# Kernel optimization log

Hardware: AMD Instinct MI355X
Metric: run time of the kernel (lower is better)

## Reference

```python
import jax, jax.numpy as jnp
import numpy as np

N_NODES = 100000
N_EDGES = 1600000
NUM_GRAPHS = 2000
IN_CH, HID = 5, 64
NEG_SLOPE = 0.2


def _lin_params(key, out_d, in_d, bias=True):
    k1, k2 = jax.random.split(key)
    bound = 1.0 / np.sqrt(in_d)
    W = jax.random.uniform(k1, (out_d, in_d), jnp.float32, -bound, bound)
    if bias:
        b = jax.random.uniform(k2, (out_d,), jnp.float32, -bound, bound)
        return W, b
    return (W,)


def setup_inputs() -> dict:
    key = jax.random.key(0)
    ks = jax.random.split(key, 12)
    x = jax.random.normal(ks[0], (N_NODES, IN_CH), jnp.float32)
    edge_index = jax.random.randint(ks[1], (2, N_EDGES), 0, N_NODES, jnp.int64)
    batch = (jnp.arange(N_NODES, dtype=jnp.int64) * NUM_GRAPHS) // N_NODES  # 50 nodes/graph, sorted
    # SAGEConv params: lin_l (on aggregated neighbors, with bias), lin_r (root, no bias)
    W1l, b1 = _lin_params(ks[2], HID, IN_CH)
    (W1r,) = _lin_params(ks[3], HID, IN_CH, bias=False)
    W2l, b2 = _lin_params(ks[4], 2 * HID, HID)
    (W2r,) = _lin_params(ks[5], 2 * HID, HID, bias=False)
    W3l, b3 = _lin_params(ks[6], 4 * HID, 2 * HID)
    (W3r,) = _lin_params(ks[7], 4 * HID, 2 * HID, bias=False)
    # classifier MLP: 512 -> 128 -> 64 -> 1
    Wc1, bc1 = _lin_params(ks[8], 2 * HID, 8 * HID)
    Wc2, bc2 = _lin_params(ks[9], HID, 2 * HID)
    Wc3, bc3 = _lin_params(ks[10], 1, HID)
    return {
        "x": x, "edge_index": edge_index, "batch": batch, "num_graphs": NUM_GRAPHS,
        "W1l": W1l, "b1": b1, "W1r": W1r,
        "W2l": W2l, "b2": b2, "W2r": W2r,
        "W3l": W3l, "b3": b3, "W3r": W3r,
        "Wc1": Wc1, "bc1": bc1, "Wc2": Wc2, "bc2": bc2, "Wc3": Wc3, "bc3": bc3,
    }


def _sage_conv(x, src, dst, Wl, b, Wr):
    # mean-aggregate messages x[src] at dst, then lin_l(agg) + lin_r(x)
    n = x.shape[0]
    s = jax.ops.segment_sum(x[src], dst, num_segments=n)
    cnt = jax.ops.segment_sum(jnp.ones((src.shape[0],), x.dtype), dst, num_segments=n)
    mean = s / jnp.maximum(cnt, 1.0)[:, None]
    return mean @ Wl.T + b + x @ Wr.T


def reference(x, edge_index, batch, num_graphs,
              W1l, b1, W1r, W2l, b2, W2r, W3l, b3, W3r,
              Wc1, bc1, Wc2, bc2, Wc3, bc3):
    src, dst = edge_index[0], edge_index[1]
    lrelu = lambda h: jax.nn.leaky_relu(h, NEG_SLOPE)
    h = lrelu(_sage_conv(x, src, dst, W1l, b1, W1r))
    h = lrelu(_sage_conv(h, src, dst, W2l, b2, W2r))
    h = lrelu(_sage_conv(h, src, dst, W3l, b3, W3r))
    # global mean + max pool per graph -> [G, 512]
    s = jax.ops.segment_sum(h, batch, num_segments=num_graphs)
    cnt = jax.ops.segment_sum(jnp.ones((h.shape[0],), h.dtype), batch, num_segments=num_graphs)
    mean_p = s / jnp.maximum(cnt, 1.0)[:, None]
    max_p = jax.ops.segment_max(h, batch, num_segments=num_graphs)
    g = jnp.concatenate([mean_p, max_p], axis=1)
    # classifier (dropout = identity in eval mode)
    g = lrelu(g @ Wc1.T + bc1)
    g = lrelu(g @ Wc2.T + bc2)
    logits = g @ Wc3.T + bc3
    return logits.squeeze(-1)
```

## Files before the change

kernel.cpp:

```cpp
#include <hip/hip_runtime.h>
#include <cstdint>
#include <cstddef>

#define NEG_SLOPE 0.2f

typedef __attribute__((ext_vector_type(8))) short bh8;
typedef __attribute__((ext_vector_type(16))) float f32x16;

__device__ inline void splitf(float x, short& hi, short& lo) {
    uint32_t u = __float_as_uint(x);
    uint32_t rh = (u + 0x7FFFu + ((u >> 16) & 1u)) & 0xFFFF0000u;
    hi = (short)(rh >> 16);
    float rem = x - __uint_as_float(rh);
    uint32_t u2 = __float_as_uint(rem);
    lo = (short)((u2 + 0x7FFFu + ((u2 >> 16) & 1u)) >> 16);
}

__device__ inline unsigned short f2bf(float x) {
    uint32_t u = __float_as_uint(x);
    return (unsigned short)((u + 0x7FFFu + ((u >> 16) & 1u)) >> 16);
}

__global__ void sentinel_kernel(float* __restrict__ out, int n) {
    int i = blockIdx.x * blockDim.x + threadIdx.x;
    if (i < n) out[i] = 12345.0f;
}

#define HIST_CH 8192
__global__ void bucket_count_kernel(const int* __restrict__ dst, int* __restrict__ bcnt,
                                    int ne, int nb) {
    __shared__ int hist[256];
    const int tid = threadIdx.x;
    hist[tid] = 0;
    __syncthreads();
    int e0 = blockIdx.x * HIST_CH;
    for (int i = tid; i < HIST_CH; i += 256) {
        int e = e0 + i;
        if (e < ne) atomicAdd(&hist[dst[e] >> 9], 1);
    }
    __syncthreads();
    if (tid < nb && hist[tid] > 0) atomicAdd(&bcnt[tid], hist[tid]);
}

__global__ void scan256_kernel(const int* __restrict__ bcnt, int* __restrict__ boff, int n) {
    const int tid = threadIdx.x, lane = tid & 63, wid = tid >> 6;
    __shared__ int wt[4];
    int v = (tid < n) ? bcnt[tid] : 0;
    int incl = v;
    #pragma unroll
    for (int o = 1; o < 64; o <<= 1) {
        int t = __shfl_up(incl, o);
        if (lane >= o) incl += t;
    }
    if (lane == 63) wt[wid] = incl;
    __syncthreads();
    if (tid < 4) {
        int w = wt[tid], winc = w;
        #pragma unroll
        for (int o = 1; o < 4; o <<= 1) {
            int t = __shfl_up(winc, o);
            if (tid >= o) winc += t;
        }
        wt[tid] = winc - w;
    }
    __syncthreads();
    int excl = wt[wid] + incl - v;
    if (tid < n) boff[tid] = excl;
    if (tid == n - 1) boff[n] = excl + v;
}

#define SCAT_CH 4096
__global__ void bucket_scatter_kernel(const int* __restrict__ src, const int* __restrict__ dst,
                                      const int* __restrict__ boff, int* __restrict__ bcur,
                                      unsigned* __restrict__ pairs, int ne, int nb) {
    __shared__ int hist[256], lcur[256], gbase[256];
    const int tid = threadIdx.x;
    hist[tid] = 0; lcur[tid] = 0;
    __syncthreads();
    int e0 = blockIdx.x * SCAT_CH;
    for (int i = tid; i < SCAT_CH; i += 256) {
        int e = e0 + i;
        if (e < ne) atomicAdd(&hist[dst[e] >> 9], 1);
    }
    __syncthreads();
    if (tid < nb) {
        int h = hist[tid];
        gbase[tid] = (h > 0) ? (boff[tid] + atomicAdd(&bcur[tid], h)) : 0;
    }
    __syncthreads();
    for (int i = tid; i < SCAT_CH; i += 256) {
        int e = e0 + i;
        if (e < ne) {
            int d = dst[e];
            int b = d >> 9;
            int r = atomicAdd(&lcur[b], 1);
            pairs[gbase[b] + r] = ((unsigned)(d & 511) << 17) | (unsigned)src[e];
        }
    }
}

__global__ __launch_bounds__(512) void bucket_sort_kernel(
        const unsigned* __restrict__ pairs, const int* __restrict__ boff,
        int* __restrict__ off, int* __restrict__ csr, int n_nodes) {
    __shared__ int cnt[512], lcur[512];
    __shared__ int wt[8];
    const int b = blockIdx.x;
    const int tid = threadIdx.x, lane = tid & 63, wid = tid >> 6;
    const int s = boff[b], t = boff[b + 1];
    cnt[tid] = 0; lcur[tid] = 0;
    __syncthreads();
    for (int i = s + tid; i < t; i += 512)
        atomicAdd(&cnt[pairs[i] >> 17], 1);
    __syncthreads();
    int v = cnt[tid];
    int incl = v;
    #pragma unroll
    for (int o = 1; o < 64; o <<= 1) {
        int tt = __shfl_up(incl, o);
        if (lane >= o) incl += tt;
    }
    if (lane == 63) wt[wid] = incl;
    __syncthreads();
    if (tid < 8) {
        int w = wt[tid], winc = w;
        #pragma unroll
        for (int o = 1; o < 8; o <<= 1) {
            int tt = __shfl_up(winc, o);
            if (tid >= o) winc += tt;
        }
        wt[tid] = winc - w;
    }
    __syncthreads();
    int excl = wt[wid] + incl - v;
    __syncthreads();
    cnt[tid] = excl;
    int node = b * 512 + tid;
    if (node < n_nodes) off[node] = s + excl;
    if (b == 0 && tid == 0) off[n_nodes] = boff[gridDim.x];
    __syncthreads();
    for (int i = s + tid; i < t; i += 512) {
        unsigned p = pairs[i];
        int bin = p >> 17;
        int r = atomicAdd(&lcur[bin], 1);
        csr[s + cnt[bin] + r] = (int)(p & 0x1FFFFu);
    }
}

__global__ void pack_wsplit_kernel(const float* __restrict__ Wl, const float* __restrict__ Wr,
                                   short* __restrict__ Whi, short* __restrict__ Wlo,
                                   int COUT, int K, int CIN) {
    int i = blockIdx.x * blockDim.x + threadIdx.x;
    if (i >= COUT * K) return;
    int n = i / K, k = i % K;
    float v = (k < CIN) ? Wl[n * CIN + k] : Wr[n * CIN + (k - CIN)];
    short h, l;
    splitf(v, h, l);
    Whi[i] = h; Wlo[i] = l;
}

__global__ __launch_bounds__(256) void sage1_kernel(
        const float* __restrict__ x, const int* __restrict__ off,
        const int* __restrict__ csr, const float* __restrict__ W1l,
        const float* __restrict__ W1r, const float* __restrict__ b1,
        float* __restrict__ h1, unsigned short* __restrict__ h1b, int n_nodes) {
    __shared__ float sWl[320], sWr[320], sb[64];
    const int tid = threadIdx.x;
    for (int i = tid; i < 320; i += 256) { sWl[i] = W1l[i]; sWr[i] = W1r[i]; }
    if (tid < 64) sb[tid] = b1[tid];
    __syncthreads();
    int node = blockIdx.x * 4 + (tid >> 6);
    int lane = tid & 63;
    if (node >= n_nodes) return;
    int slot = lane >> 3, cg = lane & 7;
    int e0 = off[node], cnt = off[node + 1] - e0;
    float a0 = 0.f, a1 = 0.f;
    int i = slot;
    for (; i + 8 < cnt; i += 16) {
        int s0 = csr[e0 + i];
        int s1 = csr[e0 + i + 8];
        a0 += (cg < 5) ? x[(size_t)s0 * 5 + cg] : 0.f;
        a1 += (cg < 5) ? x[(size_t)s1 * 5 + cg] : 0.f;
    }
    for (; i < cnt; i += 8) {
        int s = csr[e0 + i];
        a0 += (cg < 5) ? x[(size_t)s * 5 + cg] : 0.f;
    }
    float acc = a0 + a1;
    #pragma unroll
    for (int o = 8; o < 64; o <<= 1) acc += __shfl_xor(acc, o);
    float inv = (cnt > 0) ? 1.f / (float)cnt : 0.f;
    float m = acc * inv;
    float xv = (lane < 5) ? x[(size_t)node * 5 + lane] : 0.f;
    float o = sb[lane];
    #pragma unroll
    for (int c = 0; c < 5; ++c) {
        o += sWl[lane * 5 + c] * __shfl(m, c);
        o += sWr[lane * 5 + c] * __shfl(xv, c);
    }
    o = o > 0.f ? o : o * NEG_SLOPE;
    h1[(size_t)node * 64 + lane] = o;
    h1b[(size_t)node * 64 + lane] = f2bf(o);
}

template<int CIN>
__global__ void agg_bf16_kernel(const unsigned short* __restrict__ hb,
                                const int* __restrict__ off, const int* __restrict__ csr,
                                float* __restrict__ mean, int n_nodes) {
    constexpr int LPR = CIN / 8;
    constexpr int SLOTS = 64 / LPR;
    constexpr int UN = 16 / SLOTS;
    int node = blockIdx.x * (blockDim.x >> 6) + (threadIdx.x >> 6);
    int lane = threadIdx.x & 63;
    if (node >= n_nodes) return;
    int slot = lane / LPR, cg = lane % LPR;
    int e0 = off[node], cnt = off[node + 1] - e0;
    const unsigned short* base = hb + cg * 8;
    float acc[UN][8];
    #pragma unroll
    for (int u = 0; u < UN; ++u)
        #pragma unroll
        for (int k = 0; k < 8; ++k) acc[u][k] = 0.f;
    int i = slot;
    for (; i + (UN - 1) * SLOTS < cnt; i += UN * SLOTS) {
        int s[UN];
        #pragma unroll
        for (int u = 0; u < UN; ++u) s[u] = csr[e0 + i + u * SLOTS];
        uint4 v[UN];
        #pragma unroll
        for (int u = 0; u < UN; ++u)
            v[u] = *(const uint4*)(base + (size_t)s[u] * CIN);
        #pragma unroll
        for (int u = 0; u < UN; ++u) {
            unsigned w0 = v[u].x, w1 = v[u].y, w2 = v[u].z, w3 = v[u].w;
            acc[u][0] += __uint_as_float(w0 << 16);
            acc[u][1] += __uint_as_float(w0 & 0xFFFF0000u);
            acc[u][2] += __uint_as_float(w1 << 16);
            acc[u][3] += __uint_as_float(w1 & 0xFFFF0000u);
            acc[u][4] += __uint_as_float(w2 << 16);
            acc[u][5] += __uint_as_float(w2 & 0xFFFF0000u);
            acc[u][6] += __uint_as_float(w3 << 16);
            acc[u][7] += __uint_as_float(w3 & 0xFFFF0000u);
        }
    }
    for (; i < cnt; i += SLOTS) {
        uint4 v = *(const uint4*)(base + (size_t)csr[e0 + i] * CIN);
        unsigned w0 = v.x, w1 = v.y, w2 = v.z, w3 = v.w;
        acc[0][0] += __uint_as_float(w0 << 16);
        acc[0][1] += __uint_as_float(w0 & 0xFFFF0000u);
        acc[0][2] += __uint_as_float(w1 << 16);
        acc[0][3] += __uint_as_float(w1 & 0xFFFF0000u);
        acc[0][4] += __uint_as_float(w2 << 16);
        acc[0][5] += __uint_as_float(w2 & 0xFFFF0000u);
        acc[0][6] += __uint_as_float(w3 << 16);
        acc[0][7] += __uint_as_float(w3 & 0xFFFF0000u);
    }
    float r[8];
    #pragma unroll
    for (int k = 0; k < 8; ++k) {
        float s = acc[0][k];
        #pragma unroll
        for (int u = 1; u < UN; ++u) s += acc[u][k];
        r[k] = s;
    }
    #pragma unroll
    for (int o = LPR; o < 64; o <<= 1)
        #pragma unroll
        for (int k = 0; k < 8; ++k) r[k] += __shfl_xor(r[k], o);
    if (slot == 0) {
        float inv = (cnt > 0) ? 1.f / (float)cnt : 0.f;
        float4 lo = {r[0] * inv, r[1] * inv, r[2] * inv, r[3] * inv};
        float4 hi = {r[4] * inv, r[5] * inv, r[6] * inv, r[7] * inv};
        float* mp = mean + (size_t)node * CIN + cg * 8;
        *(float4*)mp = lo;
        *(float4*)(mp + 4) = hi;
    }
}

#define BM 128
#define BN 64
#define BK 16

template<bool RELU>
__global__ __launch_bounds__(256) void gemm_cat_kernel(
        const float* __restrict__ AL, const float* __restrict__ AR,
        const float* __restrict__ W, const float* __restrict__ bias,
        float* __restrict__ C, int M, int N, int K, int CIN) {
    __shared__ float As[BK][BM + 4];
    __shared__ float Bs[BK][BN + 4];
    const int row0 = blockIdx.x * BM;
    const int col0 = blockIdx.y * BN;
    const int tid = threadIdx.x;
    const int ttm = tid & 15, ttn = tid >> 4;

    float acc[8][4];
    #pragma unroll
    for (int i = 0; i < 8; ++i)
        #pragma unroll
        for (int j = 0; j < 4; ++j) acc[i][j] = 0.f;

    for (int k0 = 0; k0 < K; k0 += BK) {
        for (int i = tid; i < BM * BK; i += 256) {
            int m = i >> 4, k = i & 15;
            int r = row0 + m, kk = k0 + k;
            float v = 0.f;
            if (r < M && kk < K)
                v = (kk < CIN) ? AL[(size_t)r * CIN + kk]
                               : AR[(size_t)r * CIN + (kk - CIN)];
            As[k][m] = v;
        }
        for (int i = tid; i < BN * BK; i += 256) {
            int n = i >> 4, k = i & 15;
            int c = col0 + n, kk = k0 + k;
            Bs[k][n] = (c < N && kk < K) ? W[(size_t)c * K + kk] : 0.f;
        }
        __syncthreads();
        #pragma unroll
        for (int k = 0; k < BK; ++k) {
            float4 a0 = *(const float4*)&As[k][ttm * 8];
            float4 a1 = *(const float4*)&As[k][ttm * 8 + 4];
            float4 b0 = *(const float4*)&Bs[k][ttn * 4];
            float av[8] = {a0.x, a0.y, a0.z, a0.w, a1.x, a1.y, a1.z, a1.w};
            float bv[4] = {b0.x, b0.y, b0.z, b0.w};
            #pragma unroll
            for (int i = 0; i < 8; ++i)
                #pragma unroll
                for (int j = 0; j < 4; ++j)
                    acc[i][j] += av[i] * bv[j];
        }
        __syncthreads();
    }

    float bv[4];
    #pragma unroll
    for (int j = 0; j < 4; ++j) bv[j] = bias[col0 + ttn * 4 + j];
    #pragma unroll
    for (int i = 0; i < 8; ++i) {
        int r = row0 + ttm * 8 + i;
        if (r < M) {
            float t0 = acc[i][0] + bv[0];
            float t1 = acc[i][1] + bv[1];
            float t2 = acc[i][2] + bv[2];
            float t3 = acc[i][3] + bv[3];
            if (RELU) {
                t0 = t0 > 0.f ? t0 : t0 * NEG_SLOPE;
                t1 = t1 > 0.f ? t1 : t1 * NEG_SLOPE;
                t2 = t2 > 0.f ? t2 : t2 * NEG_SLOPE;
                t3 = t3 > 0.f ? t3 : t3 * NEG_SLOPE;
            }
            float4 v; v.x = t0; v.y = t1; v.z = t2; v.w = t3;
            *(float4*)&C[(size_t)r * N + col0 + ttn * 4] = v;
        }
    }
}

__global__ __launch_bounds__(256) void gemm_cat_mfma_kernel(
        const float* __restrict__ AL, const float* __restrict__ AR,
        const short* __restrict__ Whi, const short* __restrict__ Wlo,
        const float* __restrict__ bias, float* __restrict__ C,
        unsigned short* __restrict__ Cb16,
        int M, int N, int K, int CIN) {
    __shared__ short AsH[128][40], AsL[128][40];
    __shared__ short BsH[128][40], BsL[128][40];
    const int row0 = blockIdx.x * 128;
    const int n0 = blockIdx.y * 128;
    const int tid = threadIdx.x;
    const int w = tid >> 6;
    const int lane31 = tid & 31, lhalf = (tid & 63) >> 5;

    f32x16 acc[4];
    #pragma unroll
    for (int ci = 0; ci < 4; ++ci)
        #pragma unroll
        for (int r = 0; r < 16; ++r) acc[ci][r] = 0.f;

    for (int k0 = 0; k0 < K; k0 += 32) {
        const float* Asrc = (k0 < CIN) ? AL : AR;
        const int kb = (k0 < CIN) ? k0 : k0 - CIN;
        {
            int row = tid >> 1, kq = (tid & 1) * 16;
            int r = row0 + row;
            float vv[16];
            #pragma unroll
            for (int i = 0; i < 16; ++i) vv[i] = 0.f;
            if (r < M) {
                const float* p = &Asrc[(size_t)r * CIN + kb + kq];
                #pragma unroll
                for (int q = 0; q < 4; ++q) {
                    float4 v = ((const float4*)p)[q];
                    vv[q * 4 + 0] = v.x; vv[q * 4 + 1] = v.y;
                    vv[q * 4 + 2] = v.z; vv[q * 4 + 3] = v.w;
                }
            }
            #pragma unroll
            for (int half = 0; half < 2; ++half) {
                bh8 h8, l8;
                #pragma unroll
                for (int i = 0; i < 8; ++i) {
                    short a, b;
                    splitf(vv[half * 8 + i], a, b);
                    h8[i] = a; l8[i] = b;
                }
                *(bh8*)&AsH[row][kq + half * 8] = h8;
                *(bh8*)&AsL[row][kq + half * 8] = l8;
            }
        }
        {
            int n = tid & 127, half = tid >> 7;
            const short* src = half ? Wlo : Whi;
            const uint4* p = (const uint4*)&src[(size_t)(n0 + n) * K + k0];
            if (half) {
                #pragma unroll
                for (int q = 0; q < 4; ++q) *(uint4*)&BsL[n][q * 8] = p[q];
            } else {
                #pragma unroll
                for (int q = 0; q < 4; ++q) *(uint4*)&BsH[n][q * 8] = p[q];
            }
        }
        __syncthreads();
        #pragma unroll
        for (int ks = 0; ks < 2; ++ks) {
            int kofs = ks * 16 + lhalf * 8;
            bh8 aH = *(bh8*)&AsH[w * 32 + lane31][kofs];
            bh8 aL = *(bh8*)&AsL[w * 32 + lane31][kofs];
            #pragma unroll
            for (int ci = 0; ci < 4; ++ci) {
                bh8 bH = *(bh8*)&BsH[ci * 32 + lane31][kofs];
                bh8 bL = *(bh8*)&BsL[ci * 32 + lane31][kofs];
                acc[ci] = __builtin_amdgcn_mfma_f32_32x32x16_bf16(aH, bH, acc[ci], 0, 0, 0);
                acc[ci] = __builtin_amdgcn_mfma_f32_32x32x16_bf16(aH, bL, acc[ci], 0, 0, 0);
                acc[ci] = __builtin_amdgcn_mfma_f32_32x32x16_bf16(aL, bH, acc[ci], 0, 0, 0);
            }
        }
        __syncthreads();
    }

    #pragma unroll
    for (int ci = 0; ci < 4; ++ci) {
        int col = n0 + ci * 32 + lane31;
        float b = bias[col];
        #pragma unroll
        for (int r = 0; r < 16; ++r) {
            int row = row0 + w * 32 + (r & 3) + 8 * (r >> 2) + 4 * lhalf;
            if (row < M) {
                float v = acc[ci][r] + b;
                v = v > 0.f ? v : v * NEG_SLOPE;
                C[(size_t)row * N + col] = v;
                if (Cb16) Cb16[(size_t)row * N + col] = f2bf(v);
            }
        }
    }
}

__global__ __launch_bounds__(512) void gemm_pool_mfma2_kernel(
        const float* __restrict__ AL, const float* __restrict__ AR,
        const short* __restrict__ Whi, const short* __restrict__ Wlo,
        const float* __restrict__ bias, float* __restrict__ gout,
        int npg, int CIN, int NCH) {
    __shared__ short AsH[128][40], AsL[128][40];
    __shared__ short BsH[256][40], BsL[256][40];
    __shared__ float redS[4][258], redM[4][258];
    const int g2 = blockIdx.x * 2;
    const int K = 2 * CIN;
    const int tid = threadIdx.x;
    const int w = tid >> 6;
    const int lane31 = tid & 31, lhalf = (tid & 63) >> 5;
    const int rt = w & 3, cb = (w >> 2) * 4;

    f32x16 acc[4];
    #pragma unroll
    for (int ci = 0; ci < 4; ++ci)
        #pragma unroll
        for (int r = 0; r < 16; ++r) acc[ci][r] = 0.f;

    for (int k0 = 0; k0 < K; k0 += 32) {
        const float* Asrc = (k0 < CIN) ? AL : AR;
        const int kb = (k0 < CIN) ? k0 : k0 - CIN;
        {
            int row = tid >> 2, kq = (tid & 3) * 8;
            int grow = row >> 6, r = row & 63;
            float vv[8];
            #pragma unroll
            for (int i = 0; i < 8; ++i) vv[i] = 0.f;
            if (r < npg) {
                const float* p = &Asrc[((size_t)(g2 + grow) * npg + r) * CIN + kb + kq];
                #pragma unroll
                for (int q = 0; q < 2; ++q) {
                    float4 v = ((const float4*)p)[q];
                    vv[q * 4 + 0] = v.x; vv[q * 4 + 1] = v.y;
                    vv[q * 4 + 2] = v.z; vv[q * 4 + 3] = v.w;
                }
            }
            bh8 h8, l8;
            #pragma unroll
            for (int i = 0; i < 8; ++i) {
                short a, b;
                splitf(vv[i], a, b);
                h8[i] = a; l8[i] = b;
            }
            *(bh8*)&AsH[row][kq] = h8;
            *(bh8*)&AsL[row][kq] = l8;
        }
        {
            int n = tid & 255, half = tid >> 8;
            const short* srcw = half ? Wlo : Whi;
            const uint4* p = (const uint4*)&srcw[(size_t)n * K + k0];
            if (half) {
                #pragma unroll
                for (int q = 0; q < 4; ++q) *(uint4*)&BsL[n][q * 8] = p[q];
            } else {
                #pragma unroll
                for (int q = 0; q < 4; ++q) *(uint4*)&BsH[n][q * 8] = p[q];
            }
        }
        __syncthreads();
        #pragma unroll
        for (int ks = 0; ks < 2; ++ks) {
            int kofs = ks * 16 + lhalf * 8;
            bh8 aH = *(bh8*)&AsH[rt * 32 + lane31][kofs];
            bh8 aL = *(bh8*)&AsL[rt * 32 + lane31][kofs];
            #pragma unroll
            for (int ci = 0; ci < 4; ++ci) {
                bh8 bH = *(bh8*)&BsH[(cb + ci) * 32 + lane31][kofs];
                bh8 bL = *(bh8*)&BsL[(cb + ci) * 32 + lane31][kofs];
                acc[ci] = __builtin_amdgcn_mfma_f32_32x32x16_bf16(aH, bH, acc[ci], 0, 0, 0);
                acc[ci] = __builtin_amdgcn_mfma_f32_32x32x16_bf16(aH, bL, acc[ci], 0, 0, 0);
                acc[ci] = __builtin_amdgcn_mfma_f32_32x32x16_bf16(aL, bH, acc[ci], 0, 0, 0);
            }
        }
        __syncthreads();
    }

    #pragma unroll
    for (int ci = 0; ci < 4; ++ci) {
        int col = (cb + ci) * 32 + lane31;
        float b = bias[col];
        float ls = 0.f, lm = -__builtin_huge_valf();
        #pragma unroll
        for (int r = 0; r < 16; ++r) {
            int crow = (r & 3) + 8 * (r >> 2) + 4 * lhalf;
            int grow = (rt & 1) * 32 + crow;
            if (grow < npg) {
                float v = acc[ci][r] + b;
                v = v > 0.f ? v : v * NEG_SLOPE;
                ls += v;
                lm = fmaxf(lm, v);
            }
        }
        ls += __shfl_xor(ls, 32);
        lm = fmaxf(lm, __shfl_xor(lm, 32));
        if (lhalf == 0) { redS[rt][col] = ls; redM[rt][col] = lm; }
    }
    __syncthreads();
    {
        int c = tid & 255, gi = tid >> 8;
        float s = redS[gi * 2][c] + redS[gi * 2 + 1][c];
        float m = fmaxf(redM[gi * 2][c], redM[gi * 2 + 1][c]);
        gout[(size_t)(g2 + gi) * (2 * NCH) + c] = s / (float)npg;
        gout[(size_t)(g2 + gi) * (2 * NCH) + NCH + c] = m;
    }
}

__global__ void final_kernel(const float* __restrict__ c2, const float* __restrict__ Wc3,
                             const float* __restrict__ bc3, float* __restrict__ out, int G) {
    int g = blockIdx.x * (blockDim.x >> 6) + (threadIdx.x >> 6);
    int lane = threadIdx.x & 63;
    if (g >= G) return;
    float v = c2[(size_t)g * 64 + lane] * Wc3[lane];
    #pragma unroll
    for (int o = 32; o > 0; o >>= 1) v += __shfl_down(v, o);
    if (lane == 0) out[g] = v + bc3[0];
}

extern "C" void kernel_launch(void* const* d_in, const int* in_sizes, int n_in,
                              void* d_out, int out_size, void* d_ws, size_t ws_size,
                              hipStream_t stream) {
    const float* x   = (const float*)d_in[0];
    const int* ei    = (const int*)d_in[1];
    const float* W1l = (const float*)d_in[4];
    const float* b1  = (const float*)d_in[5];
    const float* W1r = (const float*)d_in[6];
    const float* W2l = (const float*)d_in[7];
    const float* b2  = (const float*)d_in[8];
    const float* W2r = (const float*)d_in[9];
    const float* W3l = (const float*)d_in[10];
    const float* b3  = (const float*)d_in[11];
    const float* W3r = (const float*)d_in[12];
    const float* Wc1 = (const float*)d_in[13];
    const float* bc1 = (const float*)d_in[14];
    const float* Wc2 = (const float*)d_in[15];
    const float* bc2 = (const float*)d_in[16];
    const float* Wc3 = (const float*)d_in[17];
    const float* bc3 = (const float*)d_in[18];
    float* out = (float*)d_out;

    const int nodes = in_sizes[0] / 5;
    const int ne    = in_sizes[1] / 2;
    const int G     = out_size;
    const int npg   = nodes / G;
    const int nb    = (nodes + 511) >> 9;

    char* ws = (char*)d_ws;
    size_t pos = 0;
    auto take = [&](size_t bytes) -> char* {
        char* p = ws + pos;
        pos += (bytes + 255) & ~(size_t)255;
        return p;
    };
    int* off     = (int*)take((size_t)(nodes + 1) * 4);
    int* csr     = (int*)take((size_t)ne * 4);
    int* bcnt    = (int*)take(256 * 4);
    int* bcur    = (int*)take(256 * 4);
    int* boff    = (int*)take(257 * 4);
    short* Whi2  = (short*)take((size_t)128 * 128 * 2);
    short* Wlo2  = (short*)take((size_t)128 * 128 * 2);
    short* Whi3  = (short*)take((size_t)256 * 256 * 2);
    short* Wlo3  = (short*)take((size_t)256 * 256 * 2);
    short* WhiC  = (short*)take((size_t)128 * 512 * 2);
    short* WloC  = (short*)take((size_t)128 * 512 * 2);
    float* gbuf  = (float*)take((size_t)G * 512 * 4);
    float* c1    = (float*)take((size_t)G * 128 * 4);
    float* c2    = (float*)take((size_t)G * 64 * 4);
    float* mean1 = (float*)take((size_t)nodes * 64 * 4);
    float* h1    = (float*)take((size_t)nodes * 64 * 4);
    float* h2    = (float*)take((size_t)nodes * 128 * 4);
    char* R      = take((size_t)nodes * 128 * 2);
    unsigned short* h1b = (unsigned short*)R;
    unsigned short* h2b = (unsigned short*)R;
    float* mean2 = mean1;
    unsigned* pairs = (unsigned*)mean1;

    if (pos > ws_size) {
        sentinel_kernel<<<(G + 255) / 256, 256, 0, stream>>>(out, G);
        return;
    }

    const int* src = ei;
    const int* dst = ei + ne;

    hipMemsetAsync(bcnt, 0, 512 * 4, stream);

    bucket_count_kernel<<<(ne + HIST_CH - 1) / HIST_CH, 256, 0, stream>>>(dst, bcnt, ne, nb);
    scan256_kernel<<<1, 256, 0, stream>>>(bcnt, boff, nb);
    bucket_scatter_kernel<<<(ne + SCAT_CH - 1) / SCAT_CH, 256, 0, stream>>>(
        src, dst, boff, bcur, pairs, ne, nb);
    bucket_sort_kernel<<<nb, 512, 0, stream>>>(pairs, boff, off, csr, nodes);

    pack_wsplit_kernel<<<(128 * 128 + 255) / 256, 256, 0, stream>>>(W2l, W2r, Whi2, Wlo2, 128, 128, 64);
    pack_wsplit_kernel<<<(256 * 256 + 255) / 256, 256, 0, stream>>>(W3l, W3r, Whi3, Wlo3, 256, 256, 128);
    pack_wsplit_kernel<<<(128 * 512 + 255) / 256, 256, 0, stream>>>(Wc1, Wc1, WhiC, WloC, 128, 512, 512);

    sage1_kernel<<<(nodes + 3) / 4, 256, 0, stream>>>(x, off, csr, W1l, W1r, b1, h1, h1b, nodes);

    agg_bf16_kernel<64><<<(nodes + 3) / 4, 256, 0, stream>>>(h1b, off, csr, mean1, nodes);
    {
        dim3 g((nodes + 127) / 128, 1);
        gemm_cat_mfma_kernel<<<g, 256, 0, stream>>>(mean1, h1, Whi2, Wlo2, b2, h2, h2b,
                                                    nodes, 128, 128, 64);
    }
    agg_bf16_kernel<128><<<(nodes + 3) / 4, 256, 0, stream>>>(h2b, off, csr, mean2, nodes);
    gemm_pool_mfma2_kernel<<<G / 2, 512, 0, stream>>>(mean2, h2, Whi3, Wlo3, b3, gbuf,
                                                      npg, 128, 256);
    {
        dim3 g((G + 127) / 128, 1);
        gemm_cat_mfma_kernel<<<g, 256, 0, stream>>>(gbuf, gbuf, WhiC, WloC, bc1, c1, nullptr,
                                                    G, 128, 512, 512);
    }
    {
        dim3 g((G + BM - 1) / BM, 64 / BN);
        gemm_cat_kernel<true><<<g, 256, 0, stream>>>(c1, nullptr, Wc2, bc2, c2, G, 64, 128, 128);
    }
    final_kernel<<<(G + 3) / 4, 256, 0, stream>>>(c2, Wc3, bc3, out, G);
}
```

Baseline: 407.1 us.

## Store activations as pre-split bf16 hi/lo pairs and pipeline the pooling GEMM

Node activations and neighbour means now leave each kernel as bf16 hi/lo halves instead of fp32 plus a separate bf16 copy. The MFMA GEMMs can then load them directly without splitting them into hi/lo inside the loop. This cuts global traffic and per-tile conversion ALU work. The pooling GEMM is rewritten as a templated kernel that uses a K-step of 16, prefetches the next tile into registers and reuses A/B shared memory for the reductions. A new fp32-free GEMM variant is added for layer 2. The risk is extra write instructions from unvectorized scalar short stores in the epilogues, and a changed buffer-aliasing plan.

```diff
diff --git a/kernel.cpp b/kernel.cpp
--- a/kernel.cpp
+++ b/kernel.cpp
@@ -14,11 +14,6 @@
     float rem = x - __uint_as_float(rh);
     uint32_t u2 = __float_as_uint(rem);
     lo = (short)((u2 + 0x7FFFu + ((u2 >> 16) & 1u)) >> 16);
-}
-
-__device__ inline unsigned short f2bf(float x) {
-    uint32_t u = __float_as_uint(x);
-    return (unsigned short)((u + 0x7FFFu + ((u >> 16) & 1u)) >> 16);
 }
 
 __global__ void sentinel_kernel(float* __restrict__ out, int n) {
@@ -162,7 +157,8 @@
         const float* __restrict__ x, const int* __restrict__ off,
         const int* __restrict__ csr, const float* __restrict__ W1l,
         const float* __restrict__ W1r, const float* __restrict__ b1,
-        float* __restrict__ h1, unsigned short* __restrict__ h1b, int n_nodes) {
+        unsigned short* __restrict__ h1hi, unsigned short* __restrict__ h1lo,
+        int n_nodes) {
     __shared__ float sWl[320], sWr[320], sb[64];
     const int tid = threadIdx.x;
     for (int i = tid; i < 320; i += 256) { sWl[i] = W1l[i]; sWr[i] = W1r[i]; }
@@ -198,14 +194,17 @@
         o += sWr[lane * 5 + c] * __shfl(xv, c);
     }
     o = o > 0.f ? o : o * NEG_SLOPE;
-    h1[(size_t)node * 64 + lane] = o;
-    h1b[(size_t)node * 64 + lane] = f2bf(o);
+    short h, l;
+    splitf(o, h, l);
+    h1hi[(size_t)node * 64 + lane] = (unsigned short)h;
+    h1lo[(size_t)node * 64 + lane] = (unsigned short)l;
 }
 
 template<int CIN>
 __global__ void agg_bf16_kernel(const unsigned short* __restrict__ hb,
                                 const int* __restrict__ off, const int* __restrict__ csr,
-                                float* __restrict__ mean, int n_nodes) {
+                                unsigned short* __restrict__ mhi,
+                                unsigned short* __restrict__ mlo, int n_nodes) {
     constexpr int LPR = CIN / 8;
     constexpr int SLOTS = 64 / LPR;
     constexpr int UN = 16 / SLOTS;
@@ -268,11 +267,16 @@
         for (int k = 0; k < 8; ++k) r[k] += __shfl_xor(r[k], o);
     if (slot == 0) {
         float inv = (cnt > 0) ? 1.f / (float)cnt : 0.f;
-        float4 lo = {r[0] * inv, r[1] * inv, r[2] * inv, r[3] * inv};
-        float4 hi = {r[4] * inv, r[5] * inv, r[6] * inv, r[7] * inv};
-        float* mp = mean + (size_t)node * CIN + cg * 8;
-        *(float4*)mp = lo;
-        *(float4*)(mp + 4) = hi;
+        bh8 ho, lo8;
+        #pragma unroll
+        for (int k = 0; k < 8; ++k) {
+            short a, b;
+            splitf(r[k] * inv, a, b);
+            ho[k] = a; lo8[k] = b;
+        }
+        size_t idx = (size_t)node * CIN + cg * 8;
+        *(bh8*)&mhi[idx] = ho;
+        *(bh8*)&mlo[idx] = lo8;
     }
 }
 
@@ -353,11 +357,97 @@
     }
 }
 
+__global__ __launch_bounds__(256) void gemm_cat_mfma_ps_kernel(
+        const unsigned short* __restrict__ ALhi, const unsigned short* __restrict__ ALlo,
+        const unsigned short* __restrict__ ARhi, const unsigned short* __restrict__ ARlo,
+        const short* __restrict__ Whi, const short* __restrict__ Wlo,
+        const float* __restrict__ bias,
+        unsigned short* __restrict__ Chi, unsigned short* __restrict__ Clo,
+        int M, int N, int K, int CIN) {
+    __shared__ short AsH[128][40], AsL[128][40];
+    __shared__ short BsH[128][40], BsL[128][40];
+    const int row0 = blockIdx.x * 128;
+    const int n0 = blockIdx.y * 128;
+    const int tid = threadIdx.x;
+    const int w = tid >> 6;
+    const int lane31 = tid & 31, lhalf = (tid & 63) >> 5;
+
+    f32x16 acc[4];
+    #pragma unroll
+    for (int ci = 0; ci < 4; ++ci)
+        #pragma unroll
+        for (int r = 0; r < 16; ++r) acc[ci][r] = 0.f;
+
+    for (int k0 = 0; k0 < K; k0 += 32) {
+        const unsigned short* Ahi = (k0 < CIN) ? ALhi : ARhi;
+        const unsigned short* Alo = (k0 < CIN) ? ALlo : ARlo;
+        const int kb = (k0 < CIN) ? k0 : k0 - CIN;
+        {
+            int row = tid >> 1, kq = (tid & 1) * 16;
+            int r = row0 + row;
+            uint4 h0 = {0,0,0,0}, h1v = {0,0,0,0}, l0 = {0,0,0,0}, l1 = {0,0,0,0};
+            if (r < M) {
+                const uint4* ph = (const uint4*)&Ahi[(size_t)r * CIN + kb + kq];
+                const uint4* pl = (const uint4*)&Alo[(size_t)r * CIN + kb + kq];
+                h0 = ph[0]; h1v = ph[1];
+                l0 = pl[0]; l1 = pl[1];
+            }
+            *(uint4*)&AsH[row][kq] = h0;  *(uint4*)&AsH[row][kq + 8] = h1v;
+            *(uint4*)&AsL[row][kq] = l0;  *(uint4*)&AsL[row][kq + 8] = l1;
+        }
+        {
+            int n = tid & 127, half = tid >> 7;
+            const short* src = half ? Wlo : Whi;
+            const uint4* p = (const uint4*)&src[(size_t)(n0 + n) * K + k0];
+            if (half) {
+                #pragma unroll
+                for (int q = 0; q < 4; ++q) *(uint4*)&BsL[n][q * 8] = p[q];
+            } else {
+                #pragma unroll
+                for (int q = 0; q < 4; ++q) *(uint4*)&BsH[n][q * 8] = p[q];
+            }
+        }
+        __syncthreads();
+        #pragma unroll
+        for (int ks = 0; ks < 2; ++ks) {
+            int kofs = ks * 16 + lhalf * 8;
+            bh8 aH = *(bh8*)&AsH[w * 32 + lane31][kofs];
+            bh8 aL = *(bh8*)&AsL[w * 32 + lane31][kofs];
+            #pragma unroll
+            for (int ci = 0; ci < 4; ++ci) {
+                bh8 bH = *(bh8*)&BsH[ci * 32 + lane31][kofs];
+                bh8 bL = *(bh8*)&BsL[ci * 32 + lane31][kofs];
+                acc[ci] = __builtin_amdgcn_mfma_f32_32x32x16_bf16(aH, bH, acc[ci], 0, 0, 0);
+                acc[ci] = __builtin_amdgcn_mfma_f32_32x32x16_bf16(aH, bL, acc[ci], 0, 0, 0);
+                acc[ci] = __builtin_amdgcn_mfma_f32_32x32x16_bf16(aL, bH, acc[ci], 0, 0, 0);
+            }
+        }
+        __syncthreads();
+    }
+
+    #pragma unroll
+    for (int ci = 0; ci < 4; ++ci) {
+        int col = n0 + ci * 32 + lane31;
+        float b = bias[col];
+        #pragma unroll
+        for (int r = 0; r < 16; ++r) {
+            int row = row0 + w * 32 + (r & 3) + 8 * (r >> 2) + 4 * lhalf;
+            if (row < M) {
+                float v = acc[ci][r] + b;
+                v = v > 0.f ? v : v * NEG_SLOPE;
+                short h, l;
+                splitf(v, h, l);
+                Chi[(size_t)row * N + col] = (unsigned short)h;
+                Clo[(size_t)row * N + col] = (unsigned short)l;
+            }
+        }
+    }
+}
+
 __global__ __launch_bounds__(256) void gemm_cat_mfma_kernel(
         const float* __restrict__ AL, const float* __restrict__ AR,
         const short* __restrict__ Whi, const short* __restrict__ Wlo,
         const float* __restrict__ bias, float* __restrict__ C,
-        unsigned short* __restrict__ Cb16,
         int M, int N, int K, int CIN) {
     __shared__ short AsH[128][40], AsL[128][40];
     __shared__ short BsH[128][40], BsL[128][40];
@@ -445,26 +535,30 @@
                 float v = acc[ci][r] + b;
                 v = v > 0.f ? v : v * NEG_SLOPE;
                 C[(size_t)row * N + col] = v;
-                if (Cb16) Cb16[(size_t)row * N + col] = f2bf(v);
-            }
-        }
-    }
-}
-
-__global__ __launch_bounds__(512) void gemm_pool_mfma2_kernel(
-        const float* __restrict__ AL, const float* __restrict__ AR,
+            }
+        }
+    }
+}
+
+template<int CIN>
+__global__ __launch_bounds__(512) void gemm_pool_mfma3_kernel(
+        const unsigned short* __restrict__ ALhi, const unsigned short* __restrict__ ALlo,
+        const unsigned short* __restrict__ ARhi, const unsigned short* __restrict__ ARlo,
         const short* __restrict__ Whi, const short* __restrict__ Wlo,
         const float* __restrict__ bias, float* __restrict__ gout,
-        int npg, int CIN, int NCH) {
-    __shared__ short AsH[128][40], AsL[128][40];
-    __shared__ short BsH[256][40], BsL[256][40];
-    __shared__ float redS[4][258], redM[4][258];
+        int npg, int NCH) {
+    __shared__ short AsH[128][24], AsL[128][24];
+    __shared__ short BsH[256][24], BsL[256][24];
     const int g2 = blockIdx.x * 2;
-    const int K = 2 * CIN;
+    constexpr int K = 2 * CIN;
+    constexpr int NT = K / 16;
     const int tid = threadIdx.x;
     const int w = tid >> 6;
     const int lane31 = tid & 31, lhalf = (tid & 63) >> 5;
     const int rt = w & 3, cb = (w >> 2) * 4;
+    const int arow = tid >> 2, akq = (tid & 3) * 4;
+    const int agrow = arow >> 6, ar = arow & 63;
+    const int bn = tid & 255, bhalf = tid >> 8;
 
     f32x16 acc[4];
     #pragma unroll
@@ -472,50 +566,46 @@
         #pragma unroll
         for (int r = 0; r < 16; ++r) acc[ci][r] = 0.f;
 
-    for (int k0 = 0; k0 < K; k0 += 32) {
-        const float* Asrc = (k0 < CIN) ? AL : AR;
-        const int kb = (k0 < CIN) ? k0 : k0 - CIN;
+    const size_t abase = ((size_t)(g2 + agrow) * npg + ar) * CIN + akq;
+    const short* srcw = bhalf ? Wlo : Whi;
+
+    uint2 cAh = {0,0}, cAl = {0,0};
+    uint4 cB0, cB1;
+    {
+        if (ar < npg) {
+            cAh = *(const uint2*)&ALhi[abase];
+            cAl = *(const uint2*)&ALlo[abase];
+        }
+        const uint4* pb = (const uint4*)&srcw[(size_t)bn * K];
+        cB0 = pb[0]; cB1 = pb[1];
+    }
+
+    #pragma unroll
+    for (int t = 0; t < NT; ++t) {
+        *(uint2*)&AsH[arow][akq] = cAh;
+        *(uint2*)&AsL[arow][akq] = cAl;
+        if (bhalf) {
+            *(uint4*)&BsL[bn][0] = cB0; *(uint4*)&BsL[bn][8] = cB1;
+        } else {
+            *(uint4*)&BsH[bn][0] = cB0; *(uint4*)&BsH[bn][8] = cB1;
+        }
+        __syncthreads();
+        uint2 nAh = {0,0}, nAl = {0,0};
+        uint4 nB0 = {0,0,0,0}, nB1 = {0,0,0,0};
+        if (t + 1 < NT) {
+            const int k0 = (t + 1) * 16;
+            const unsigned short* Ahi = (k0 < CIN) ? ALhi : ARhi;
+            const unsigned short* Alo = (k0 < CIN) ? ALlo : ARlo;
+            const int kb = (k0 < CIN) ? k0 : k0 - CIN;
+            if (ar < npg) {
+                nAh = *(const uint2*)&Ahi[abase + kb];
+                nAl = *(const uint2*)&Alo[abase + kb];
+            }
+            const uint4* pb = (const uint4*)&srcw[(size_t)bn * K + k0];
+            nB0 = pb[0]; nB1 = pb[1];
+        }
         {
-            int row = tid >> 2, kq = (tid & 3) * 8;
-            int grow = row >> 6, r = row & 63;
-            float vv[8];
-            #pragma unroll
-            for (int i = 0; i < 8; ++i) vv[i] = 0.f;
-            if (r < npg) {
-                const float* p = &Asrc[((size_t)(g2 + grow) * npg + r) * CIN + kb + kq];
-                #pragma unroll
-                for (int q = 0; q < 2; ++q) {
-                    float4 v = ((const float4*)p)[q];
-                    vv[q * 4 + 0] = v.x; vv[q * 4 + 1] = v.y;
-                    vv[q * 4 + 2] = v.z; vv[q * 4 + 3] = v.w;
-                }
-            }
-            bh8 h8, l8;
-            #pragma unroll
-            for (int i = 0; i < 8; ++i) {
-                short a, b;
-                splitf(vv[i], a, b);
-                h8[i] = a; l8[i] = b;
-            }
-            *(bh8*)&AsH[row][kq] = h8;
-            *(bh8*)&AsL[row][kq] = l8;
-        }
-        {
-            int n = tid & 255, half = tid >> 8;
-            const short* srcw = half ? Wlo : Whi;
-            const uint4* p = (const uint4*)&srcw[(size_t)n * K + k0];
-            if (half) {
-                #pragma unroll
-                for (int q = 0; q < 4; ++q) *(uint4*)&BsL[n][q * 8] = p[q];
-            } else {
-                #pragma unroll
-                for (int q = 0; q < 4; ++q) *(uint4*)&BsH[n][q * 8] = p[q];
-            }
-        }
-        __syncthreads();
-        #pragma unroll
-        for (int ks = 0; ks < 2; ++ks) {
-            int kofs = ks * 16 + lhalf * 8;
+            int kofs = lhalf * 8;
             bh8 aH = *(bh8*)&AsH[rt * 32 + lane31][kofs];
             bh8 aL = *(bh8*)&AsL[rt * 32 + lane31][kofs];
             #pragma unroll
@@ -528,7 +618,11 @@
             }
         }
         __syncthreads();
-    }
+        if (t + 1 < NT) { cAh = nAh; cAl = nAl; cB0 = nB0; cB1 = nB1; }
+    }
+
+    float (*redS)[258] = (float(*)[258])&AsH[0][0];
+    float (*redM)[258] = (float(*)[258])&AsL[0][0];
 
     #pragma unroll
     for (int ci = 0; ci < 4; ++ci) {
@@ -620,14 +714,15 @@
     float* gbuf  = (float*)take((size_t)G * 512 * 4);
     float* c1    = (float*)take((size_t)G * 128 * 4);
     float* c2    = (float*)take((size_t)G * 64 * 4);
-    float* mean1 = (float*)take((size_t)nodes * 64 * 4);
-    float* h1    = (float*)take((size_t)nodes * 64 * 4);
-    float* h2    = (float*)take((size_t)nodes * 128 * 4);
-    char* R      = take((size_t)nodes * 128 * 2);
-    unsigned short* h1b = (unsigned short*)R;
-    unsigned short* h2b = (unsigned short*)R;
-    float* mean2 = mean1;
-    unsigned* pairs = (unsigned*)mean1;
+    unsigned short* m1hi = (unsigned short*)take((size_t)nodes * 64 * 2);
+    unsigned short* m1lo = (unsigned short*)take((size_t)nodes * 64 * 2);
+    unsigned short* h1hi = (unsigned short*)take((size_t)nodes * 64 * 2);
+    unsigned short* h1lo = (unsigned short*)take((size_t)nodes * 64 * 2);
+    unsigned short* h2hi = (unsigned short*)take((size_t)nodes * 128 * 2);
+    unsigned short* h2lo = (unsigned short*)take((size_t)nodes * 128 * 2);
+    unsigned short* m2hi = m1hi;
+    unsigned short* m2lo = h1hi;
+    unsigned* pairs = (unsigned*)m1hi;
 
     if (pos > ws_size) {
         sentinel_kernel<<<(G + 255) / 256, 256, 0, stream>>>(out, G);
@@ -649,20 +744,22 @@
     pack_wsplit_kernel<<<(256 * 256 + 255) / 256, 256, 0, stream>>>(W3l, W3r, Whi3, Wlo3, 256, 256, 128);
     pack_wsplit_kernel<<<(128 * 512 + 255) / 256, 256, 0, stream>>>(Wc1, Wc1, WhiC, WloC, 128, 512, 512);
 
-    sage1_kernel<<<(nodes + 3) / 4, 256, 0, stream>>>(x, off, csr, W1l, W1r, b1, h1, h1b, nodes);
-
-    agg_bf16_kernel<64><<<(nodes + 3) / 4, 256, 0, stream>>>(h1b, off, csr, mean1, nodes);
+    sage1_kernel<<<(nodes + 3) / 4, 256, 0, stream>>>(x, off, csr, W1l, W1r, b1,
+                                                      h1hi, h1lo, nodes);
+
+    agg_bf16_kernel<64><<<(nodes + 3) / 4, 256, 0, stream>>>(h1hi, off, csr, m1hi, m1lo, nodes);
     {
         dim3 g((nodes + 127) / 128, 1);
-        gemm_cat_mfma_kernel<<<g, 256, 0, stream>>>(mean1, h1, Whi2, Wlo2, b2, h2, h2b,
-                                                    nodes, 128, 128, 64);
-    }
-    agg_bf16_kernel<128><<<(nodes + 3) / 4, 256, 0, stream>>>(h2b, off, csr, mean2, nodes);
-    gemm_pool_mfma2_kernel<<<G / 2, 512, 0, stream>>>(mean2, h2, Whi3, Wlo3, b3, gbuf,
-                                                      npg, 128, 256);
+        gemm_cat_mfma_ps_kernel<<<g, 256, 0, stream>>>(m1hi, m1lo, h1hi, h1lo,
+                                                       Whi2, Wlo2, b2, h2hi, h2lo,
+                                                       nodes, 128, 128, 64);
+    }
+    agg_bf16_kernel<128><<<(nodes + 3) / 4, 256, 0, stream>>>(h2hi, off, csr, m2hi, m2lo, nodes);
+    gemm_pool_mfma3_kernel<128><<<G / 2, 512, 0, stream>>>(m2hi, m2lo, h2hi, h2lo,
+                                                           Whi3, Wlo3, b3, gbuf, npg, 256);
     {
         dim3 g((G + 127) / 128, 1);
-        gemm_cat_mfma_kernel<<<g, 256, 0, stream>>>(gbuf, gbuf, WhiC, WloC, bc1, c1, nullptr,
+        gemm_cat_mfma_kernel<<<g, 256, 0, stream>>>(gbuf, gbuf, WhiC, WloC, bc1, c1,
                                                     G, 128, 512, 512);
     }
     {
```

Result: faster. 395.3 us (median of 2 runs) (-2.9%).
